# Optimization experiments

Hardware: AMD Instinct MI355X
Metric: run time of the kernel (lower is better)

Reference implementation:

```python
import jax, jax.numpy as jnp
import numpy as np


def setup_inputs() -> dict:
    key = jax.random.key(0)
    k1, k2, k3 = jax.random.split(key, 3)
    x1 = jax.random.normal(k1, (6, 3, 256, 256), dtype=jnp.float32)
    # ConvTranspose2d(3,3,1) weight layout in torch is (in_ch, out_ch, 1, 1); squeeze to (in, out)
    W = jax.random.normal(k2, (3, 3), dtype=jnp.float32) * 0.3
    b = jax.random.normal(k3, (3,), dtype=jnp.float32) * 0.1
    return {"x1": x1, "W": W, "b": b}


def reference(x1, W, b):
    # 1x1 transposed conv == per-pixel channel mix: y[b,o,h,w] = sum_i x[b,i,h,w] * W[i,o] + b[o]
    v1 = jnp.einsum('bihw,io->bohw', x1, W) + b[None, :, None, None]
    v2 = v1 + 3.0
    v3 = v2 * 3.0
    v4 = jax.nn.relu(v3)
    v5 = v4 + 3.0
    v6 = jax.nn.relu(v5)
    v7 = v6 * 3.0
    v8 = v7 + 3.0
    v10 = jnp.tile(v6, (1, 3, 1, 1))           # [B,9,H,W]
    v11 = jnp.tile(v2, (1, 3, 1, 1))           # [B,9,H,W]
    v12 = jnp.transpose(v11, (0, 1, 3, 2))     # [B,9,W,H]
    v13 = jnp.transpose(v10, (0, 2, 1, 3))     # [B,H,9,W]
    v14 = v7 - 3.0
    v15 = jax.nn.relu(v14)
    v16 = v15 - 3.0
    v17 = jax.nn.relu(v16)
    v18 = v17 - 3.0
    v19 = jax.nn.relu(v18)
    v20 = v19 - 3.0
    v21 = v20 - 3.0
    v24 = jnp.tile(v12, (1, 1, 1, 3))          # [B,9,W,3H]
    v25 = jnp.tile(v13, (1, 1, 1, 3))          # [B,H,9,3W]
    v26 = jnp.transpose(v24, (0, 3, 1, 2))     # [B,3H,9,W]
    v28 = jnp.transpose(v25, (0, 3, 1, 2))     # [B,3W,H,9]
    v30 = jnp.tile(v26, (1, 1, 1, 3))          # [B,3H,9,3W]
    v33 = jnp.tile(v28, (1, 1, 1, 3))          # [B,3W,H,27]
    v37 = jnp.tile(v30, (2, 1, 1, 1))          # [2B,3H,9,3W]
    v42 = jnp.split(v24, 3, axis=0)            # chunk(3) along batch
    v43 = jnp.split(v25, 3, axis=0)
    v46 = jnp.concatenate(v42, axis=1)         # [B/3,27,W,3H]
    v47 = jnp.concatenate(v43, axis=3)         # [B/3,H,9,9W]
    m1 = jnp.max(v37, axis=0)                  # [3H,9,3W] = [768,9,768]
    out = (m1 + jnp.max(v46) + jnp.min(v47) + jnp.max(v8)
           + jnp.min(v21) + jnp.min(v33))
    return out
```

## Files before the change

### kernel.cpp

```cpp
#include <hip/hip_runtime.h>

static constexpr int NPIX = 256 * 256;

typedef float f4 __attribute__((ext_vector_type(4)));

__device__ __forceinline__ float chain_v6(float v2) {
    return fmaxf(fmaxf(3.0f * v2, 0.0f) + 3.0f, 0.0f);
}
__device__ __forceinline__ float chain_v21(float v2) {
    float t = 3.0f * chain_v6(v2);
    t = fmaxf(t - 3.0f, 0.0f);
    t = fmaxf(t - 3.0f, 0.0f);
    t = fmaxf(t - 3.0f, 0.0f);
    return t - 6.0f;
}

__global__ __launch_bounds__(256) void k_compute(const float* __restrict__ x,
                                                 const float* __restrict__ Wp,
                                                 const float* __restrict__ bp,
                                                 float* __restrict__ M,
                                                 float2* __restrict__ partials) {
    const int t = threadIdx.x;
    const int p = blockIdx.x * 256 + t;
    const int lane = t & 63, wid = t >> 6;

    float W[9];
#pragma unroll
    for (int i = 0; i < 9; ++i) W[i] = Wp[i];
    const float bias[3] = {bp[0], bp[1], bp[2]};

    float Mc[3] = {-3.4e38f, -3.4e38f, -3.4e38f};
    float minv2 = 3.4e38f;

#pragma unroll
    for (int b = 0; b < 6; ++b) {
        const float x0 = __builtin_nontemporal_load(&x[(b * 3 + 0) * NPIX + p]);
        const float x1 = __builtin_nontemporal_load(&x[(b * 3 + 1) * NPIX + p]);
        const float x2 = __builtin_nontemporal_load(&x[(b * 3 + 2) * NPIX + p]);
#pragma unroll
        for (int c = 0; c < 3; ++c) {
            float v2 = fmaf(x0, W[c], fmaf(x1, W[3 + c], fmaf(x2, W[6 + c], bias[c] + 3.0f)));
            Mc[c] = fmaxf(Mc[c], v2);
            minv2 = fminf(minv2, v2);
        }
    }

    M[0 * NPIX + p] = Mc[0];
    M[1 * NPIX + p] = Mc[1];
    M[2 * NPIX + p] = Mc[2];

    float maxv2 = fmaxf(Mc[0], fmaxf(Mc[1], Mc[2]));
#pragma unroll
    for (int o = 32; o > 0; o >>= 1) {
        maxv2 = fmaxf(maxv2, __shfl_down(maxv2, o));
        minv2 = fminf(minv2, __shfl_down(minv2, o));
    }
    __shared__ float smx[4], smn[4];
    if (lane == 0) { smx[wid] = maxv2; smn[wid] = minv2; }
    __syncthreads();
    if (t == 0) {
        partials[blockIdx.x] =
            make_float2(fmaxf(fmaxf(smx[0], smx[1]), fmaxf(smx[2], smx[3])),
                        fminf(fminf(smn[0], smn[1]), fminf(smn[2], smn[3])));
    }
}

__global__ __launch_bounds__(192) void k_out(const f4* __restrict__ Mv,
                                             const float2* __restrict__ partials,
                                             f4* __restrict__ out) {
    const int t = threadIdx.x;
    const int lane = t & 63, wid = t >> 6;

    float2 pr = partials[t];
    float A = pr.x, B = pr.y;
    if (t < 64) {
        float2 q = partials[192 + t];
        A = fmaxf(A, q.x);
        B = fminf(B, q.y);
    }
#pragma unroll
    for (int o = 32; o > 0; o >>= 1) {
        A = fmaxf(A, __shfl_down(A, o));
        B = fminf(B, __shfl_down(B, o));
    }
    __shared__ float sA[3], sB[3];
    if (lane == 0) { sA[wid] = A; sB[wid] = B; }
    __syncthreads();
    const float Ag = fmaxf(sA[0], fmaxf(sA[1], sA[2]));
    const float Bg = fminf(sB[0], fminf(sB[1], sB[2]));
    const float S = Ag + 2.0f * chain_v6(Bg) + (3.0f * chain_v6(Ag) + 3.0f) + chain_v21(Bg);

    const int c = blockIdx.x;
    const int xr = blockIdx.y;

    const f4 m = Mv[c * (NPIX / 4) + (xr & 255) * 64 + (t & 63)];
    const f4 r = m + S;
    const int base = (xr * 9 + c) * 192 + t;
    __builtin_nontemporal_store(r, &out[base]);
    __builtin_nontemporal_store(r, &out[base + 576]);
    __builtin_nontemporal_store(r, &out[base + 1152]);
}

extern "C" void kernel_launch(void* const* d_in, const int* in_sizes, int n_in,
                              void* d_out, int out_size, void* d_ws, size_t ws_size,
                              hipStream_t stream) {
    const float* x = (const float*)d_in[0];
    const float* W = (const float*)d_in[1];
    const float* b = (const float*)d_in[2];

    float* M = (float*)d_ws;
    float2* partials = (float2*)((char*)d_ws + 3 * NPIX * 4);

    hipLaunchKernelGGL(k_compute, dim3(NPIX / 256), dim3(256), 0, stream, x, W, b, M, partials);
    hipLaunchKernelGGL(k_out, dim3(3, 768), dim3(192), 0, stream, (const f4*)M, partials, (f4*)d_out);
}
```

Baseline: 15.08 us.

## Vectorize compute kernel to float4 and restructure output kernel grid

The compute kernel now processes four pixels per thread with float4 nontemporal loads and stores, using 128 blocks of 128 threads instead of 256 blocks of 256. The output kernel collapses its 2D grid into 768 blocks. Each block now covers all three channels (one wave per channel) and issues nine stores per thread, and only the first wave reduces the 128 partials before broadcasting through shared memory. The aim is wider memory transactions and fewer blocks doing redundant global reductions, at the cost of much lower parallelism in the compute kernel (only 128 blocks on a large GPU).

Result: no change. 15.10 us (+0.1%).

```diff
diff --git a/kernel.cpp b/kernel.cpp
--- a/kernel.cpp
+++ b/kernel.cpp
@@ -1,6 +1,7 @@
 #include <hip/hip_runtime.h>
 
 static constexpr int NPIX = 256 * 256;
+static constexpr int NF4 = NPIX / 4;
 
 typedef float f4 __attribute__((ext_vector_type(4)));
 
@@ -15,13 +16,20 @@
     return t - 6.0f;
 }
 
-__global__ __launch_bounds__(256) void k_compute(const float* __restrict__ x,
+__device__ __forceinline__ f4 vmax(f4 a, f4 b) {
+    return f4{fmaxf(a.x, b.x), fmaxf(a.y, b.y), fmaxf(a.z, b.z), fmaxf(a.w, b.w)};
+}
+__device__ __forceinline__ f4 vmin(f4 a, f4 b) {
+    return f4{fminf(a.x, b.x), fminf(a.y, b.y), fminf(a.z, b.z), fminf(a.w, b.w)};
+}
+
+__global__ __launch_bounds__(128) void k_compute(const f4* __restrict__ x,
                                                  const float* __restrict__ Wp,
                                                  const float* __restrict__ bp,
-                                                 float* __restrict__ M,
+                                                 f4* __restrict__ Mv,
                                                  float2* __restrict__ partials) {
     const int t = threadIdx.x;
-    const int p = blockIdx.x * 256 + t;
+    const int p4 = blockIdx.x * 128 + t;
     const int lane = t & 63, wid = t >> 6;
 
     float W[9];
@@ -29,39 +37,42 @@
     for (int i = 0; i < 9; ++i) W[i] = Wp[i];
     const float bias[3] = {bp[0], bp[1], bp[2]};
 
-    float Mc[3] = {-3.4e38f, -3.4e38f, -3.4e38f};
-    float minv2 = 3.4e38f;
+    f4 Mc[3];
+#pragma unroll
+    for (int c = 0; c < 3; ++c) Mc[c] = f4{-3.4e38f, -3.4e38f, -3.4e38f, -3.4e38f};
+    f4 mn = f4{3.4e38f, 3.4e38f, 3.4e38f, 3.4e38f};
 
 #pragma unroll
     for (int b = 0; b < 6; ++b) {
-        const float x0 = __builtin_nontemporal_load(&x[(b * 3 + 0) * NPIX + p]);
-        const float x1 = __builtin_nontemporal_load(&x[(b * 3 + 1) * NPIX + p]);
-        const float x2 = __builtin_nontemporal_load(&x[(b * 3 + 2) * NPIX + p]);
+        const f4 x0 = __builtin_nontemporal_load(&x[(b * 3 + 0) * NF4 + p4]);
+        const f4 x1 = __builtin_nontemporal_load(&x[(b * 3 + 1) * NF4 + p4]);
+        const f4 x2 = __builtin_nontemporal_load(&x[(b * 3 + 2) * NF4 + p4]);
 #pragma unroll
         for (int c = 0; c < 3; ++c) {
-            float v2 = fmaf(x0, W[c], fmaf(x1, W[3 + c], fmaf(x2, W[6 + c], bias[c] + 3.0f)));
-            Mc[c] = fmaxf(Mc[c], v2);
-            minv2 = fminf(minv2, v2);
+            f4 v2 = x0 * W[c] + x1 * W[3 + c] + x2 * W[6 + c] + (bias[c] + 3.0f);
+            Mc[c] = vmax(Mc[c], v2);
+            mn = vmin(mn, v2);
         }
     }
 
-    M[0 * NPIX + p] = Mc[0];
-    M[1 * NPIX + p] = Mc[1];
-    M[2 * NPIX + p] = Mc[2];
+    Mv[0 * NF4 + p4] = Mc[0];
+    Mv[1 * NF4 + p4] = Mc[1];
+    Mv[2 * NF4 + p4] = Mc[2];
 
-    float maxv2 = fmaxf(Mc[0], fmaxf(Mc[1], Mc[2]));
+    f4 mx4 = vmax(Mc[0], vmax(Mc[1], Mc[2]));
+    float maxv2 = fmaxf(fmaxf(mx4.x, mx4.y), fmaxf(mx4.z, mx4.w));
+    float minv2 = fminf(fminf(mn.x, mn.y), fminf(mn.z, mn.w));
+
 #pragma unroll
     for (int o = 32; o > 0; o >>= 1) {
         maxv2 = fmaxf(maxv2, __shfl_down(maxv2, o));
         minv2 = fminf(minv2, __shfl_down(minv2, o));
     }
-    __shared__ float smx[4], smn[4];
+    __shared__ float smx[2], smn[2];
     if (lane == 0) { smx[wid] = maxv2; smn[wid] = minv2; }
     __syncthreads();
     if (t == 0) {
-        partials[blockIdx.x] =
-            make_float2(fmaxf(fmaxf(smx[0], smx[1]), fmaxf(smx[2], smx[3])),
-                        fminf(fminf(smn[0], smn[1]), fminf(smn[2], smn[3])));
+        partials[blockIdx.x] = make_float2(fmaxf(smx[0], smx[1]), fminf(smn[0], smn[1]));
     }
 }
 
@@ -69,48 +80,48 @@
                                              const float2* __restrict__ partials,
                                              f4* __restrict__ out) {
     const int t = threadIdx.x;
-    const int lane = t & 63, wid = t >> 6;
+    __shared__ float sS;
 
-    float2 pr = partials[t];
-    float A = pr.x, B = pr.y;
     if (t < 64) {
-        float2 q = partials[192 + t];
-        A = fmaxf(A, q.x);
-        B = fminf(B, q.y);
+        float2 p0 = partials[t];
+        float2 p1 = partials[t + 64];
+        float A = fmaxf(p0.x, p1.x), B = fminf(p0.y, p1.y);
+#pragma unroll
+        for (int o = 32; o > 0; o >>= 1) {
+            A = fmaxf(A, __shfl_down(A, o));
+            B = fminf(B, __shfl_down(B, o));
+        }
+        if (t == 0) {
+            sS = A + 2.0f * chain_v6(B) + (3.0f * chain_v6(A) + 3.0f) + chain_v21(B);
+        }
     }
+    __syncthreads();
+    const float S = sS;
+
+    const int c = t >> 6, l = t & 63;
+    const int xr = blockIdx.x;
+
+    const f4 r = Mv[c * NF4 + (xr & 255) * 64 + l] + S;
+    const int base = (xr * 9 + c) * 192 + l;
 #pragma unroll
-    for (int o = 32; o > 0; o >>= 1) {
-        A = fmaxf(A, __shfl_down(A, o));
-        B = fminf(B, __shfl_down(B, o));
+    for (int k = 0; k < 3; ++k) {
+#pragma unroll
+        for (int w = 0; w < 3; ++w) {
+            __builtin_nontemporal_store(r, &out[base + k * 576 + w * 64]);
+        }
     }
-    __shared__ float sA[3], sB[3];
-    if (lane == 0) { sA[wid] = A; sB[wid] = B; }
-    __syncthreads();
-    const float Ag = fmaxf(sA[0], fmaxf(sA[1], sA[2]));
-    const float Bg = fminf(sB[0], fminf(sB[1], sB[2]));
-    const float S = Ag + 2.0f * chain_v6(Bg) + (3.0f * chain_v6(Ag) + 3.0f) + chain_v21(Bg);
-
-    const int c = blockIdx.x;
-    const int xr = blockIdx.y;
-
-    const f4 m = Mv[c * (NPIX / 4) + (xr & 255) * 64 + (t & 63)];
-    const f4 r = m + S;
-    const int base = (xr * 9 + c) * 192 + t;
-    __builtin_nontemporal_store(r, &out[base]);
-    __builtin_nontemporal_store(r, &out[base + 576]);
-    __builtin_nontemporal_store(r, &out[base + 1152]);
 }
 
 extern "C" void kernel_launch(void* const* d_in, const int* in_sizes, int n_in,
                               void* d_out, int out_size, void* d_ws, size_t ws_size,
                               hipStream_t stream) {
-    const float* x = (const float*)d_in[0];
+    const f4* x = (const f4*)d_in[0];
     const float* W = (const float*)d_in[1];
     const float* b = (const float*)d_in[2];
 
-    float* M = (float*)d_ws;
+    f4* Mv = (f4*)d_ws;
     float2* partials = (float2*)((char*)d_ws + 3 * NPIX * 4);
 
-    hipLaunchKernelGGL(k_compute, dim3(NPIX / 256), dim3(256), 0, stream, x, W, b, M, partials);
-    hipLaunchKernelGGL(k_out, dim3(3, 768), dim3(192), 0, stream, (const f4*)M, partials, (f4*)d_out);
+    hipLaunchKernelGGL(k_compute, dim3(128), dim3(128), 0, stream, x, W, b, Mv, partials);
+    hipLaunchKernelGGL(k_out, dim3(768), dim3(192), 0, stream, Mv, partials, (f4*)d_out);
 }
```
